# Optimization experiments

Hardware: AMD Instinct MI355X
Metric: run time of the kernel (lower is better)

## Reference

```python
import jax, jax.numpy as jnp
import numpy as np

N_NODES = 20000
N_EDGES = 160000
N_GRAPHS = 64
EMB_DIM = 16
N_BASIS = 16
MAX_RADIUS = 5.0
MUL_IN = 8   # output_size: multiplicity of scalar atom features
MUL_OUT = 4  # multiplicity per output irrep (4x0e + 4x1o + 4x2e -> dim 36)
W_NUMEL = 3 * MUL_IN * MUL_IN * MUL_OUT  # 768 per-edge tensor-product weights


def setup_inputs() -> dict:
    key = jax.random.key(0)
    ks = jax.random.split(key, 16)
    pos = jax.random.normal(ks[0], (N_NODES, 3), jnp.float32) * 3.0
    A = jax.random.randint(ks[1], (N_NODES,), 0, 10)
    batch = jnp.sort(jax.random.randint(ks[2], (N_NODES,), 0, N_GRAPHS))
    edge_src = jax.random.randint(ks[3], (N_EDGES,), 0, N_NODES)
    edge_dst = jax.random.randint(ks[4], (N_EDGES,), 0, N_NODES)
    edge_shifts = jnp.zeros((N_EDGES, 3), jnp.float32)
    cell = jnp.broadcast_to(jnp.eye(3, dtype=jnp.float32) * 10.0, (N_GRAPHS, 3, 3))
    emb_table = jax.random.normal(ks[5], (10, EMB_DIM), jnp.float32)
    fit_w1 = jax.random.normal(ks[6], (EMB_DIM, 64), jnp.float32) * (2.0 / EMB_DIM) ** 0.5
    fit_b1 = jnp.zeros((64,), jnp.float32)
    fit_w2 = jax.random.normal(ks[7], (64, 32), jnp.float32) * (2.0 / 64.0) ** 0.5
    fit_b2 = jnp.zeros((32,), jnp.float32)
    fit_w3 = jax.random.normal(ks[8], (32, MUL_IN), jnp.float32) * (2.0 / 32.0) ** 0.5
    fit_b3 = jnp.zeros((MUL_IN,), jnp.float32)
    fc_w1 = jax.random.normal(ks[9], (N_BASIS, 64), jnp.float32)
    fc_w2 = jax.random.normal(ks[10], (64, 64), jnp.float32)
    fc_w3 = jax.random.normal(ks[11], (64, 64), jnp.float32)
    fc_w4 = jax.random.normal(ks[12], (64, W_NUMEL), jnp.float32)
    return dict(pos=pos, A=A, batch=batch, edge_src=edge_src, edge_dst=edge_dst,
                edge_shifts=edge_shifts, cell=cell, emb_table=emb_table,
                fit_w1=fit_w1, fit_b1=fit_b1, fit_w2=fit_w2, fit_b2=fit_b2,
                fit_w3=fit_w3, fit_b3=fit_b3,
                fc_w1=fc_w1, fc_w2=fc_w2, fc_w3=fc_w3, fc_w4=fc_w4)


def _forward(pos, edge_shifts, cell, emb_table, fit_w1, fit_b1, fit_w2, fit_b2,
             fit_w3, fit_b3, fc_w1, fc_w2, fc_w3, fc_w4, A, batch, edge_src, edge_dst):
    E = edge_src.shape[0]
    # edge vectors with periodic shifts
    shift = jnp.einsum('ni,nij->nj', edge_shifts, cell[batch[edge_src]])
    ev = pos[edge_dst] - pos[edge_src] + shift                     # [E,3]
    r = jnp.sqrt(jnp.sum(ev * ev, axis=1))                         # [E]
    v = ev / jnp.maximum(r, 1e-9)[:, None]
    x, y, z = v[:, 0], v[:, 1], v[:, 2]
    # spherical harmonics lmax=2, normalize=True, 'component' normalization (e3nn order)
    sh0 = jnp.ones_like(x)                                         # [E]
    sh1 = jnp.sqrt(3.0) * jnp.stack([y, z, x], axis=-1)            # [E,3]
    s15 = jnp.sqrt(15.0); s5 = jnp.sqrt(5.0)
    sh2 = jnp.stack([s15 * x * y, s15 * y * z, (s5 / 2.0) * (3.0 * z * z - 1.0),
                     s15 * x * z, (s15 / 2.0) * (x * x - y * y)], axis=-1)  # [E,5]
    # node scalar features: embedding + fitnet MLP (SiLU)
    h = jax.nn.silu(emb_table[A] @ fit_w1 + fit_b1)
    h = jax.nn.silu(h @ fit_w2 + fit_b2)
    Ai = h @ fit_w3 + fit_b3                                       # [N, MUL_IN]
    # soft_one_hot_linspace(gaussian, cutoff=True) * sqrt(n_basis)
    centers = jnp.linspace(0.0, MAX_RADIUS, N_BASIS + 2)[1:-1]
    step = centers[1] - centers[0]
    rb = jnp.exp(-(((r[:, None] - centers) / step) ** 2)) / 1.12 * jnp.sqrt(jnp.float32(N_BASIS))
    # radial net -> per-edge tensor-product weights (e3nn FullyConnectedNet style, no bias)
    g = jax.nn.silu(rb @ fc_w1 / jnp.sqrt(jnp.float32(N_BASIS)))
    g = jax.nn.silu(g @ fc_w2 / 8.0)
    g = jax.nn.silu(g @ fc_w3 / 8.0)
    w = (g @ fc_w4 / 8.0).reshape(E, 3, MUL_IN, MUL_IN, MUL_OUT)   # [E,3 paths,u,v,w]
    # FullTensorProduct(Ai_src, sh) then FullyConnectedTensorProduct(., Ai_dst) with
    # per-edge weights; scalar x irrep paths factorize: out_l[e,w,m] = S_l[e,w]*sh_l[e,m]
    P = Ai[edge_src][:, :, None] * Ai[edge_dst][:, None, :]        # [E,u,v]
    S = jnp.einsum('euv,eluvw->elw', P, w) / jnp.float32(MUL_IN)   # path norm 1/sqrt(u*v)
    out0 = S[:, 0, :] * sh0[:, None]                               # [E,4]
    out1 = (S[:, 1, :, None] * sh1[:, None, :]).reshape(E, MUL_OUT * 3)
    out2 = (S[:, 2, :, None] * sh2[:, None, :]).reshape(E, MUL_OUT * 5)
    ef = jnp.concatenate([out0, out1, out2], axis=-1)              # [E,36]
    # scatter-mean to destination nodes
    cnt = jnp.clip(jax.ops.segment_sum(jnp.ones((E,), ef.dtype), edge_dst,
                                       num_segments=N_NODES), 1.0)
    return jax.ops.segment_sum(ef, edge_dst, num_segments=N_NODES) / cnt[:, None]


def reference(pos, A, batch, edge_src, edge_dst, edge_shifts, cell, emb_table,
              fit_w1, fit_b1, fit_w2, fit_b2, fit_w3, fit_b3,
              fc_w1, fc_w2, fc_w3, fc_w4):
    return _forward(pos, edge_shifts, cell, emb_table, fit_w1, fit_b1, fit_w2,
                    fit_b2, fit_w3, fit_b3, fc_w1, fc_w2, fc_w3, fc_w4,
                    A, batch, edge_src, edge_dst)
```

## Files before the change

### kernel.cpp

```cpp
#include <hip/hip_runtime.h>
#include <math.h>

#define N_NODES 20000
#define N_EDGES 160000

#define NBINS   512
#define BINS1   513
#define RMAX    7.5f

static const size_t OFF_EF  = 0;
static const size_t OFF_T   = OFF_EF  + (size_t)N_EDGES * 16 * 4;
static const size_t OFF_G   = OFF_T   + (size_t)100 * 64 * 12 * 4;
static const size_t OFF_SV  = OFF_G   + (size_t)64 * BINS1 * 4;
static const size_t OFF_NOFF= OFF_SV  + (size_t)100 * BINS1 * 12 * 4;
static const size_t OFF_NCNT= OFF_NOFF+ (size_t)(N_NODES + 1) * 4;
static const size_t OFF_NCUR= OFF_NCNT+ (size_t)N_NODES * 4;

#define P1_T_BLOCKS  25
#define P1_G_BLOCKS  9
#define P1_H_BLOCKS  625
#define P1_GRID (P1_T_BLOCKS + P1_G_BLOCKS + P1_H_BLOCKS)
#define P2_CHUNKS 2
#define P2_GRID (1 + 100 * P2_CHUNKS)

__device__ __forceinline__ float silu_f(float x) {
    return x / (1.0f + __expf(-x));
}

__global__ __launch_bounds__(256) void prep1_kernel(
        const float* __restrict__ emb,
        const float* __restrict__ fw1, const float* __restrict__ fb1,
        const float* __restrict__ fw2, const float* __restrict__ fb2,
        const float* __restrict__ fw3, const float* __restrict__ fb3,
        const float* __restrict__ fc_w1, const float* __restrict__ fc_w2,
        const float* __restrict__ fc_w3, const float* __restrict__ fc_w4,
        const int* __restrict__ edst,
        float* __restrict__ T, float* __restrict__ g_tT,
        int* __restrict__ cnt_i) {
    __shared__ float smem[4096];
    int b = blockIdx.x;
    int tid = threadIdx.x;

    if (b < P1_T_BLOCKS) {
        float* h1s = smem;
        float* h2s = smem + 640;
        float* ai  = smem + 960;
        for (int idx = tid; idx < 640; idx += 256) {
            int t = idx >> 6, j = idx & 63;
            float acc = fb1[j];
            #pragma unroll
            for (int i = 0; i < 16; i++) acc += emb[t * 16 + i] * fw1[i * 64 + j];
            h1s[idx] = silu_f(acc);
        }
        __syncthreads();
        for (int idx = tid; idx < 320; idx += 256) {
            int t = idx >> 5, j = idx & 31;
            float acc = fb2[j];
            #pragma unroll
            for (int i = 0; i < 64; i++) acc += h1s[t * 64 + i] * fw2[i * 32 + j];
            h2s[idx] = silu_f(acc);
        }
        __syncthreads();
        if (tid < 80) {
            int t = tid >> 3, j = tid & 7;
            float acc = fb3[j];
            #pragma unroll
            for (int i = 0; i < 32; i++) acc += h2s[t * 32 + i] * fw3[i * 8 + j];
            ai[tid] = acc;
        }
        __syncthreads();

        int idx = b * 256 + tid;
        int pair = idx >> 6;
        int k = idx & 63;
        int ts = pair / 10, td = pair - ts * 10;
        float a[8], bb[8];
        #pragma unroll
        for (int i = 0; i < 8; i++) a[i] = ai[ts * 8 + i];
        #pragma unroll
        for (int i = 0; i < 8; i++) bb[i] = ai[td * 8 + i];
        float sv[12];
        #pragma unroll
        for (int i = 0; i < 12; i++) sv[i] = 0.0f;
        const float* wk = fc_w4 + k * 768;
        #pragma unroll 2
        for (int u = 0; u < 8; u++) {
            #pragma unroll
            for (int v = 0; v < 8; v++) {
                float ab = a[u] * bb[v];
                const float* wp = wk + u * 32 + v * 4;
                float4 w0 = *(const float4*)(wp);
                float4 w1 = *(const float4*)(wp + 256);
                float4 w2 = *(const float4*)(wp + 512);
                sv[0] += ab * w0.x; sv[1] += ab * w0.y; sv[2]  += ab * w0.z; sv[3]  += ab * w0.w;
                sv[4] += ab * w1.x; sv[5] += ab * w1.y; sv[6]  += ab * w1.z; sv[7]  += ab * w1.w;
                sv[8] += ab * w2.x; sv[9] += ab * w2.y; sv[10] += ab * w2.z; sv[11] += ab * w2.w;
            }
        }
        float* tp = T + pair * 768 + k * 12;
        #pragma unroll
        for (int j = 0; j < 12; j++) tp[j] = sv[j];
    } else if (b < P1_T_BLOCKS + P1_G_BLOCKS) {
        int lane = tid & 63;
        int wq = __builtin_amdgcn_readfirstlane(tid >> 6);
        int bin = (b - P1_T_BLOCKS) * 64 + lane;
        bool valid = (bin <= NBINS);
        float r = (float)bin * (RMAX / (float)NBINS);

        float rb[16];
        const float step = 5.0f / 17.0f;
        const float istep = 17.0f / 5.0f;
        const float rsc = 4.0f / 1.12f;
        #pragma unroll
        for (int i = 0; i < 16; i++) {
            float dd = (r - (float)(i + 1) * step) * istep;
            rb[i] = __expf(-dd * dd) * rsc;
        }

        #pragma unroll
        for (int jj = 0; jj < 16; jj++) {
            int j = wq * 16 + jj;
            float a0 = 0, a1 = 0, a2 = 0, a3 = 0;
            #pragma unroll
            for (int i = 0; i < 16; i += 4) {
                a0 += rb[i]     * fc_w1[(i)     * 64 + j];
                a1 += rb[i + 1] * fc_w1[(i + 1) * 64 + j];
                a2 += rb[i + 2] * fc_w1[(i + 2) * 64 + j];
                a3 += rb[i + 3] * fc_w1[(i + 3) * 64 + j];
            }
            smem[j * 64 + lane] = silu_f(((a0 + a1) + (a2 + a3)) * 0.25f);
        }
        __syncthreads();

        float acc[16];
        #pragma unroll
        for (int jj = 0; jj < 16; jj++) acc[jj] = 0.0f;
        #pragma unroll
        for (int c = 0; c < 4; c++) {
            float hc[16];
            #pragma unroll
            for (int i = 0; i < 16; i++) hc[i] = smem[(c * 16 + i) * 64 + lane];
            #pragma unroll
            for (int jj = 0; jj < 16; jj++) {
                int j = wq * 16 + jj;
                #pragma unroll
                for (int i = 0; i < 16; i++) acc[jj] += hc[i] * fc_w2[(c * 16 + i) * 64 + j];
            }
        }
        __syncthreads();
        #pragma unroll
        for (int jj = 0; jj < 16; jj++) smem[(wq * 16 + jj) * 64 + lane] = silu_f(acc[jj] * 0.125f);
        __syncthreads();

        #pragma unroll
        for (int jj = 0; jj < 16; jj++) acc[jj] = 0.0f;
        #pragma unroll
        for (int c = 0; c < 4; c++) {
            float hc[16];
            #pragma unroll
            for (int i = 0; i < 16; i++) hc[i] = smem[(c * 16 + i) * 64 + lane];
            #pragma unroll
            for (int jj = 0; jj < 16; jj++) {
                int j = wq * 16 + jj;
                #pragma unroll
                for (int i = 0; i < 16; i++) acc[jj] += hc[i] * fc_w3[(c * 16 + i) * 64 + j];
            }
        }
        if (valid) {
            #pragma unroll
            for (int jj = 0; jj < 16; jj++)
                g_tT[(size_t)(wq * 16 + jj) * BINS1 + bin] = silu_f(acc[jj] * 0.125f);
        }
    } else {
        int e = (b - P1_T_BLOCKS - P1_G_BLOCKS) * 256 + tid;
        if (e < N_EDGES) atomicAdd(&cnt_i[edst[e]], 1);
    }
}

__global__ __launch_bounds__(256) void prep2_kernel(
        const int* __restrict__ cnt_i, int* __restrict__ node_off,
        const float* __restrict__ T, const float* __restrict__ g_tT,
        float* __restrict__ sv_table) {
    __shared__ int part[256];
    int b = blockIdx.x;
    int tid = threadIdx.x;

    if (b == 0) {
        int base = tid * 79;
        int s = 0;
        for (int i = 0; i < 79; i++) {
            int n = base + i;
            if (n < N_NODES) s += cnt_i[n];
        }
        part[tid] = s;
        __syncthreads();
        for (int off = 1; off < 256; off <<= 1) {
            int v = part[tid];
            int add = (tid >= off) ? part[tid - off] : 0;
            __syncthreads();
            part[tid] = v + add;
            __syncthreads();
        }
        int run = (tid == 0) ? 0 : part[tid - 1];
        for (int i = 0; i < 79; i++) {
            int n = base + i;
            if (n < N_NODES) { node_off[n] = run; run += cnt_i[n]; }
        }
        if (tid == 255) node_off[N_NODES] = part[255];
        return;
    }

    int idx = b - 1;
    int pair = idx / P2_CHUNKS;
    int chunk = idx - pair * P2_CHUNKS;
    int b0 = chunk * 512 + tid;
    int b1 = b0 + 256;
    bool v0 = (b0 <= NBINS), v1 = (b1 <= NBINS);
    int rb0 = v0 ? b0 : NBINS;
    int rb1 = v1 ? b1 : NBINS;

    float acc0[12], acc1[12];
    #pragma unroll
    for (int j = 0; j < 12; j++) { acc0[j] = 0.0f; acc1[j] = 0.0f; }
    const float* Tp = T + pair * 768;
    #pragma unroll 4
    for (int k = 0; k < 64; k++) {
        float g0 = g_tT[(size_t)k * BINS1 + rb0];
        float g1 = g_tT[(size_t)k * BINS1 + rb1];
        const float* tr = Tp + k * 12;
        float4 t0 = *(const float4*)(tr);
        float4 t1 = *(const float4*)(tr + 4);
        float4 t2 = *(const float4*)(tr + 8);
        acc0[0] += g0 * t0.x; acc0[1] += g0 * t0.y; acc0[2]  += g0 * t0.z; acc0[3]  += g0 * t0.w;
        acc0[4] += g0 * t1.x; acc0[5] += g0 * t1.y; acc0[6]  += g0 * t1.z; acc0[7]  += g0 * t1.w;
        acc0[8] += g0 * t2.x; acc0[9] += g0 * t2.y; acc0[10] += g0 * t2.z; acc0[11] += g0 * t2.w;
        acc1[0] += g1 * t0.x; acc1[1] += g1 * t0.y; acc1[2]  += g1 * t0.z; acc1[3]  += g1 * t0.w;
        acc1[4] += g1 * t1.x; acc1[5] += g1 * t1.y; acc1[6]  += g1 * t1.z; acc1[7]  += g1 * t1.w;
        acc1[8] += g1 * t2.x; acc1[9] += g1 * t2.y; acc1[10] += g1 * t2.z; acc1[11] += g1 * t2.w;
    }
    const float isc = 1.0f / 64.0f;
    if (v0) {
        float* o = sv_table + ((size_t)pair * BINS1 + b0) * 12;
        #pragma unroll
        for (int j = 0; j < 12; j++) o[j] = acc0[j] * isc;
    }
    if (v1) {
        float* o = sv_table + ((size_t)pair * BINS1 + b1) * 12;
        #pragma unroll
        for (int j = 0; j < 12; j++) o[j] = acc1[j] * isc;
    }
}

__global__ __launch_bounds__(256) void edge_table_kernel(
        const float* __restrict__ pos, const int* __restrict__ batch,
        const int* __restrict__ esrc, const int* __restrict__ edst,
        const float* __restrict__ shifts, const float* __restrict__ cell,
        const int* __restrict__ A,
        const int* __restrict__ node_off, int* __restrict__ node_cur,
        const float* __restrict__ sv_table, float* __restrict__ ef) {
    int e = blockIdx.x * 256 + threadIdx.x;
    if (e >= N_EDGES) return;

    int s = esrc[e], d = edst[e];
    int slot = atomicAdd(&node_cur[d], 1);
    int base = node_off[d];

    int gb = batch[s];
    float t0 = shifts[e * 3 + 0], t1 = shifts[e * 3 + 1], t2 = shifts[e * 3 + 2];
    const float* C = cell + gb * 9;
    float shx = t0 * C[0] + t1 * C[3] + t2 * C[6];
    float shy = t0 * C[1] + t1 * C[4] + t2 * C[7];
    float shz = t0 * C[2] + t1 * C[5] + t2 * C[8];
    float ex = pos[d * 3 + 0] - pos[s * 3 + 0] + shx;
    float ey = pos[d * 3 + 1] - pos[s * 3 + 1] + shy;
    float ez = pos[d * 3 + 2] - pos[s * 3 + 2] + shz;
    float r = sqrtf(ex * ex + ey * ey + ez * ez);
    float inv = 1.0f / fmaxf(r, 1e-9f);
    float x = ex * inv, y = ey * inv, z = ez * inv;

    float sv[12];
    if (r >= RMAX) {
        #pragma unroll
        for (int j = 0; j < 12; j++) sv[j] = 0.0f;
    } else {
        int pair = A[s] * 10 + A[d];
        float t = r * ((float)NBINS / RMAX);
        int i = (int)t;
        i = (i > NBINS - 1) ? (NBINS - 1) : i;
        float f = t - (float)i;
        const float* r0 = sv_table + ((size_t)pair * BINS1 + i) * 12;
        #pragma unroll
        for (int j = 0; j < 12; j++) {
            float lo = r0[j], hi = r0[12 + j];
            sv[j] = lo + f * (hi - lo);
        }
    }

    float4* dst = (float4*)(ef + (size_t)(base + slot) * 16);
    dst[0] = make_float4(sv[0], sv[1], sv[2],  sv[3]);
    dst[1] = make_float4(sv[4], sv[5], sv[6],  sv[7]);
    dst[2] = make_float4(sv[8], sv[9], sv[10], sv[11]);
    dst[3] = make_float4(x, y, z, 0.0f);
}

__global__ __launch_bounds__(256) void gather_kernel(const float* __restrict__ ef,
                                                     const int* __restrict__ node_off,
                                                     float* __restrict__ out) {
    int t = blockIdx.x * 256 + threadIdx.x;
    if (t >= N_NODES * 4) return;
    int n = t >> 2;
    int q = t & 3;
    int beg = node_off[n], end = node_off[n + 1];
    const float4* ef4 = (const float4*)ef;

    const float S3  = 1.7320508075688772f;
    const float S15 = 3.8729833462074170f;
    const float S5  = 2.2360679774997896f;

    float acc[36];
    #pragma unroll
    for (int j = 0; j < 36; j++) acc[j] = 0.0f;

    for (int p = beg + q; p < end; p += 4) {
        const float4* rp = ef4 + (size_t)p * 4;
        float4 svA = rp[0];
        float4 svB = rp[1];
        float4 svC = rp[2];
        float4 dv  = rp[3];
        float x = dv.x, y = dv.y, z = dv.z;
        float sh1v[3] = { S3 * y, S3 * z, S3 * x };
        float sh2v[5] = { S15 * x * y, S15 * y * z, 0.5f * S5 * (3.0f * z * z - 1.0f),
                          S15 * x * z, 0.5f * S15 * (x * x - y * y) };
        acc[0] += svA.x; acc[1] += svA.y; acc[2] += svA.z; acc[3] += svA.w;
        float bw[4] = { svB.x, svB.y, svB.z, svB.w };
        #pragma unroll
        for (int w = 0; w < 4; w++) {
            #pragma unroll
            for (int j = 0; j < 3; j++) acc[4 + w * 3 + j] += bw[w] * sh1v[j];
        }
        float cw[4] = { svC.x, svC.y, svC.z, svC.w };
        #pragma unroll
        for (int w = 0; w < 4; w++) {
            #pragma unroll
            for (int j = 0; j < 5; j++) acc[16 + w * 5 + j] += cw[w] * sh2v[j];
        }
    }

    #pragma unroll
    for (int j = 0; j < 36; j++) {
        acc[j] += __shfl_xor(acc[j], 1);
        acc[j] += __shfl_xor(acc[j], 2);
    }

    if (q == 0) {
        float c = 1.0f / fmaxf((float)(end - beg), 1.0f);
        float4* o4 = (float4*)out + (size_t)n * 9;
        #pragma unroll
        for (int k = 0; k < 9; k++)
            o4[k] = make_float4(acc[k * 4 + 0] * c, acc[k * 4 + 1] * c,
                                acc[k * 4 + 2] * c, acc[k * 4 + 3] * c);
    }
}

extern "C" void kernel_launch(void* const* d_in, const int* in_sizes, int n_in,
                              void* d_out, int out_size, void* d_ws, size_t ws_size,
                              hipStream_t stream) {
    const float* pos    = (const float*)d_in[0];
    const int*   A      = (const int*)d_in[1];
    const int*   batch  = (const int*)d_in[2];
    const int*   esrc   = (const int*)d_in[3];
    const int*   edst   = (const int*)d_in[4];
    const float* shifts = (const float*)d_in[5];
    const float* cell   = (const float*)d_in[6];
    const float* emb    = (const float*)d_in[7];
    const float* fw1    = (const float*)d_in[8];
    const float* fb1    = (const float*)d_in[9];
    const float* fw2    = (const float*)d_in[10];
    const float* fb2    = (const float*)d_in[11];
    const float* fw3    = (const float*)d_in[12];
    const float* fb3    = (const float*)d_in[13];
    const float* fcw1   = (const float*)d_in[14];
    const float* fcw2   = (const float*)d_in[15];
    const float* fcw3   = (const float*)d_in[16];
    const float* fcw4   = (const float*)d_in[17];
    float* out = (float*)d_out;

    char* ws = (char*)d_ws;
    float* ef      = (float*)(ws + OFF_EF);
    float* T       = (float*)(ws + OFF_T);
    float* g_tT    = (float*)(ws + OFF_G);
    float* sv_table= (float*)(ws + OFF_SV);
    int*   node_off= (int*)(ws + OFF_NOFF);
    int*   cnt_i   = (int*)(ws + OFF_NCNT);
    int*   node_cur= (int*)(ws + OFF_NCUR);

    hipMemsetAsync(cnt_i, 0, (size_t)2 * N_NODES * 4, stream);

    prep1_kernel<<<P1_GRID, 256, 0, stream>>>(emb, fw1, fb1, fw2, fb2, fw3, fb3,
                                              fcw1, fcw2, fcw3, fcw4, edst,
                                              T, g_tT, cnt_i);
    prep2_kernel<<<P2_GRID, 256, 0, stream>>>(cnt_i, node_off, T, g_tT, sv_table);
    edge_table_kernel<<<(N_EDGES + 255) / 256, 256, 0, stream>>>(
        pos, batch, esrc, edst, shifts, cell, A, node_off, node_cur, sv_table, ef);
    gather_kernel<<<(N_NODES * 4 + 255) / 256, 256, 0, stream>>>(ef, node_off, out);
}
```

Before: 191.0 us.

## Split prep2 table build across more blocks with k-split waves and LDS reduction

The per-pair sv_table build now uses 9 chunks of 64 bins instead of 2 chunks of 512 bins. Each of the four waves in a block handles 16 of the 64 k terms, and the partial sums are reduced through shared memory. T is staged in LDS, and the output is written with coalesced stores. This raises block count and parallelism in a small kernel that previously launched only 201 blocks. The cost is an extra LDS reduction and two barriers per block.

```diff
diff --git a/kernel.cpp b/kernel.cpp
--- a/kernel.cpp
+++ b/kernel.cpp
@@ -20,7 +20,7 @@
 #define P1_G_BLOCKS  9
 #define P1_H_BLOCKS  625
 #define P1_GRID (P1_T_BLOCKS + P1_G_BLOCKS + P1_H_BLOCKS)
-#define P2_CHUNKS 2
+#define P2_CHUNKS 9
 #define P2_GRID (1 + 100 * P2_CHUNKS)
 
 __device__ __forceinline__ float silu_f(float x) {
@@ -181,11 +181,12 @@
         const int* __restrict__ cnt_i, int* __restrict__ node_off,
         const float* __restrict__ T, const float* __restrict__ g_tT,
         float* __restrict__ sv_table) {
-    __shared__ int part[256];
+    __shared__ float smem[4096];
     int b = blockIdx.x;
     int tid = threadIdx.x;
 
     if (b == 0) {
+        int* part = (int*)smem;
         int base = tid * 79;
         int s = 0;
         for (int i = 0; i < 79; i++) {
@@ -213,41 +214,52 @@
     int idx = b - 1;
     int pair = idx / P2_CHUNKS;
     int chunk = idx - pair * P2_CHUNKS;
-    int b0 = chunk * 512 + tid;
-    int b1 = b0 + 256;
-    bool v0 = (b0 <= NBINS), v1 = (b1 <= NBINS);
-    int rb0 = v0 ? b0 : NBINS;
-    int rb1 = v1 ? b1 : NBINS;
-
-    float acc0[12], acc1[12];
-    #pragma unroll
-    for (int j = 0; j < 12; j++) { acc0[j] = 0.0f; acc1[j] = 0.0f; }
+
+    float* part = smem;
+    float* Tlds = smem + 3328;
+
     const float* Tp = T + pair * 768;
-    #pragma unroll 4
-    for (int k = 0; k < 64; k++) {
-        float g0 = g_tT[(size_t)k * BINS1 + rb0];
-        float g1 = g_tT[(size_t)k * BINS1 + rb1];
-        const float* tr = Tp + k * 12;
-        float4 t0 = *(const float4*)(tr);
-        float4 t1 = *(const float4*)(tr + 4);
-        float4 t2 = *(const float4*)(tr + 8);
-        acc0[0] += g0 * t0.x; acc0[1] += g0 * t0.y; acc0[2]  += g0 * t0.z; acc0[3]  += g0 * t0.w;
-        acc0[4] += g0 * t1.x; acc0[5] += g0 * t1.y; acc0[6]  += g0 * t1.z; acc0[7]  += g0 * t1.w;
-        acc0[8] += g0 * t2.x; acc0[9] += g0 * t2.y; acc0[10] += g0 * t2.z; acc0[11] += g0 * t2.w;
-        acc1[0] += g1 * t0.x; acc1[1] += g1 * t0.y; acc1[2]  += g1 * t0.z; acc1[3]  += g1 * t0.w;
-        acc1[4] += g1 * t1.x; acc1[5] += g1 * t1.y; acc1[6]  += g1 * t1.z; acc1[7]  += g1 * t1.w;
-        acc1[8] += g1 * t2.x; acc1[9] += g1 * t2.y; acc1[10] += g1 * t2.z; acc1[11] += g1 * t2.w;
-    }
+    #pragma unroll
+    for (int i = tid; i < 768; i += 256) Tlds[i] = Tp[i];
+    __syncthreads();
+
+    int lane = tid & 63;
+    int wq = tid >> 6;
+    int bin = chunk * 64 + lane;
+    bool valid = (bin <= NBINS);
+    int rb = valid ? bin : NBINS;
+
+    float acc[12];
+    #pragma unroll
+    for (int j = 0; j < 12; j++) acc[j] = 0.0f;
+    #pragma unroll
+    for (int kk = 0; kk < 16; kk++) {
+        int k = wq * 16 + kk;
+        float g = g_tT[(size_t)k * BINS1 + rb];
+        const float* Tl = Tlds + k * 12;
+        #pragma unroll
+        for (int j = 0; j < 12; j++) acc[j] += g * Tl[j];
+    }
+
+    float* pp = part + (size_t)wq * 64 * 13 + (size_t)lane * 13;
+    #pragma unroll
+    for (int j = 0; j < 12; j++) pp[j] = acc[j];
+    __syncthreads();
+
     const float isc = 1.0f / 64.0f;
-    if (v0) {
-        float* o = sv_table + ((size_t)pair * BINS1 + b0) * 12;
-        #pragma unroll
-        for (int j = 0; j < 12; j++) o[j] = acc0[j] * isc;
-    }
-    if (v1) {
-        float* o = sv_table + ((size_t)pair * BINS1 + b1) * 12;
-        #pragma unroll
-        for (int j = 0; j < 12; j++) o[j] = acc1[j] * isc;
+    float* svp = sv_table + (size_t)pair * BINS1 * 12 + (size_t)chunk * 64 * 12;
+    #pragma unroll
+    for (int i = 0; i < 3; i++) {
+        int o = tid + 256 * i;
+        int bl = o / 12;
+        int j = o - bl * 12;
+        if (chunk * 64 + bl <= NBINS) {
+            float s = part[(size_t)0 * 832 + bl * 13 + j]
+                    + part[(size_t)1 * 832 + bl * 13 + j]
+                    + part[(size_t)2 * 832 + bl * 13 + j]
+                    + part[(size_t)3 * 832 + bl * 13 + j];
+            svp[o] = s * isc;
+        }
     }
 }
 
```

After: 191.2 us. About the same (+0.1%).
